# Optimization experiments

Hardware: AMD Instinct MI355X
Metric: run time of the kernel (lower is better)

## Reference

```python
import jax, jax.numpy as jnp
import numpy as np

N_GRAPHS = 2000
NODES_PER_GRAPH = 50
EDGES_PER_GRAPH = 800  # avg degree 16
N_NODES = N_GRAPHS * NODES_PER_GRAPH          # 100_000
N_EDGES = N_GRAPHS * EDGES_PER_GRAPH          # 1_600_000
F_IN, F_H, F_PRED = 64, 128, 512
N_STEPS = 3


def _glorot(key, shape):
    fan_in, fan_out = shape[0], shape[1]
    scale = jnp.sqrt(2.0 / (fan_in + fan_out)).astype(jnp.float32)
    return jax.random.normal(key, shape, dtype=jnp.float32) * scale


def setup_inputs() -> dict:
    key = jax.random.key(0)
    ks = jax.random.split(key, 12)
    node_features = jax.random.normal(ks[0], (N_NODES, F_IN), dtype=jnp.float32)
    edge_features = jax.random.normal(ks[1], (N_EDGES, 4), dtype=jnp.float32)  # unused by model
    # edges stay within their own graph: local ids in [0, NODES_PER_GRAPH) + graph offset
    offs = (jnp.arange(N_GRAPHS, dtype=jnp.int32) * NODES_PER_GRAPH)[:, None]  # [G,1]
    src = (jax.random.randint(ks[2], (N_GRAPHS, EDGES_PER_GRAPH), 0, NODES_PER_GRAPH, dtype=jnp.int32) + offs).reshape(-1)
    dst = (jax.random.randint(ks[3], (N_GRAPHS, EDGES_PER_GRAPH), 0, NODES_PER_GRAPH, dtype=jnp.int32) + offs).reshape(-1)
    pair_indices = jnp.stack([src, dst], axis=0)  # [2, E]
    num_nodes = jnp.full((N_GRAPHS,), NODES_PER_GRAPH, dtype=jnp.int32)
    num_edges = jnp.full((N_GRAPHS,), EDGES_PER_GRAPH, dtype=jnp.int32)
    # GCN weights: [F_IN->F_H, F_H->F_H, F_H->F_H]
    W0 = _glorot(ks[4], (F_IN, F_H)); b0 = jnp.zeros((F_H,), jnp.float32)
    W1 = _glorot(ks[5], (F_H, F_H)); b1 = jnp.zeros((F_H,), jnp.float32)
    W2 = _glorot(ks[6], (F_H, F_H)); b2 = jnp.zeros((F_H,), jnp.float32)
    Wp1 = _glorot(ks[7], (F_H, F_PRED)); bp1 = jnp.zeros((F_PRED,), jnp.float32)
    Wp2 = _glorot(ks[8], (F_PRED, 1)); bp2 = jnp.zeros((1,), jnp.float32)
    return dict(node_features=node_features, edge_features=edge_features,
                pair_indices=pair_indices, num_nodes=num_nodes, num_edges=num_edges,
                W0=W0, b0=b0, W1=W1, b1=b1, W2=W2, b2=b2,
                Wp1=Wp1, bp1=bp1, Wp2=Wp2, bp2=bp2)


def reference(node_features, edge_features, pair_indices, num_nodes, num_edges,
              W0, b0, W1, b1, W2, b2, Wp1, bp1, Wp2, bp2):
    N = node_features.shape[0]
    G = num_nodes.shape[0]
    src, dst = pair_indices[0], pair_indices[1]
    ones_e = jnp.ones(src.shape[0], dtype=jnp.float32)
    # DGL GraphConv norm='both': D_out^{-1/2} on source side, D_in^{-1/2} on dest side, degrees clamped >= 1
    deg_out = jax.ops.segment_sum(ones_e, src, num_segments=N)
    deg_in = jax.ops.segment_sum(ones_e, dst, num_segments=N)
    norm_out = jnp.clip(deg_out, 1.0) ** -0.5  # [N]
    norm_in = jnp.clip(deg_in, 1.0) ** -0.5    # [N]

    def gcn_conv(feat, W, b):
        h = (feat * norm_out[:, None]) @ W                       # [N, F_out] (W applied pre-aggregation)
        agg = jax.ops.segment_sum(h[src], dst, num_segments=N)   # neighbor sum
        return jax.nn.relu(agg * norm_in[:, None] + b)

    x = gcn_conv(node_features, W0, b0)
    x = gcn_conv(x, W1, b1)
    x = gcn_conv(x, W2, b2)  # [N, F_H]

    # AvgPooling: per-graph mean over nodes
    graph_ids = jnp.repeat(jnp.arange(G, dtype=jnp.int32), num_nodes, total_repeat_length=N)
    sums = jax.ops.segment_sum(x, graph_ids, num_segments=G)       # [G, F_H]
    means = sums / num_nodes.astype(x.dtype)[:, None]

    h = jax.nn.relu(means @ Wp1 + bp1)   # Dense(512, relu)
    out = h @ Wp2 + bp2                  # Dense(1, linear) -> [G, 1]
    return out
```

## Files before the change

### kernel.cpp

```cpp
#include <hip/hip_runtime.h>

#define NG   2000
#define NPG  50
#define EPG  800
#define F0   64
#define FH   128
#define FP   512

typedef __attribute__((ext_vector_type(8))) short  short8;
typedef __attribute__((ext_vector_type(8))) __bf16 bf16x8;
typedef __attribute__((ext_vector_type(4))) float  f32x4;
typedef unsigned short u16;
typedef unsigned int   u32;

__device__ inline u16 bf16_rne(float x) {
    u32 u = __builtin_bit_cast(u32, x);
    u += 0x7fffu + ((u >> 16) & 1u);
    return (u16)(u >> 16);
}
__device__ inline float bf16f(u16 h) {
    u32 u = ((u32)h) << 16;
    return __builtin_bit_cast(float, u);
}
__device__ inline u32 cvtpk2(float lo, float hi) {
    u32 r;
    asm("v_cvt_pk_bf16_f32 %0, %1, %2" : "=v"(r) : "v"(lo), "v"(hi));
    return r;
}
__device__ inline void split2(float v0, float v1, u32& hp, u32& lp) {
    hp = cvtpk2(v0, v1);
    float h0 = __builtin_bit_cast(float, hp << 16);
    float h1 = __builtin_bit_cast(float, hp & 0xffff0000u);
    lp = cvtpk2(v0 - h0, v1 - h1);
}
__device__ inline f32x4 mfma16(short8 a, short8 b, f32x4 c) {
    return __builtin_amdgcn_mfma_f32_16x16x32_bf16(
        __builtin_bit_cast(bf16x8, a), __builtin_bit_cast(bf16x8, b), c, 0, 0, 0);
}

__device__ inline int xb_idx(int row, int col) { return row * 128 + (col ^ ((row & 7) << 3)); }
__device__ inline int cn_idx(int d, int s)     { return d * 64  + (s   ^ ((d   & 7) << 3)); }

__global__ __launch_bounds__(256) void pack_w(
    const float* __restrict__ W0, const float* __restrict__ W1,
    const float* __restrict__ W2, u16* __restrict__ WpH, u16* __restrict__ WpL)
{
    int t = blockIdx.x * 256 + threadIdx.x;
    if (t >= 80 * 64) return;
    int fid = t >> 6, lane = t & 63;
    const float* W; int nsub, kstep;
    if (fid < 16)      { W = W0; int r = fid;      nsub = r >> 1; kstep = r & 1; }
    else if (fid < 48) { W = W1; int r = fid - 16; nsub = r >> 2; kstep = r & 3; }
    else               { W = W2; int r = fid - 48; nsub = r >> 2; kstep = r & 3; }
    int n  = nsub * 16 + (lane & 15);
    int kb = kstep * 32 + (lane >> 4) * 8;
    size_t off = (size_t)fid * 512 + (size_t)lane * 8;
#pragma unroll
    for (int i = 0; i < 8; ++i) {
        float v = W[(size_t)(kb + i) * FH + n];
        u16 h = bf16_rne(v);
        WpH[off + i] = h;
        WpL[off + i] = bf16_rne(v - bf16f(h));
    }
}

template<int KST, bool LAST>
__device__ void layer_fn(const u16* __restrict__ WpH, const u16* __restrict__ WpL,
                         int fid0, const float* __restrict__ bias,
                         u16* XbH, u16* XbL,
                         const short8 (&aReg)[4][2],
                         float* pool, const float* nin64, const float* nout64,
                         int lane, int nsg)
{
    const int l15 = lane & 15, lk = lane >> 4;
    const int feat = nsg * 16 + l15;
    const float bc = bias[feat];

    f32x4 acc[4];
#pragma unroll
    for (int ms = 0; ms < 4; ++ms) acc[ms] = f32x4{0.f, 0.f, 0.f, 0.f};
#pragma unroll
    for (int ks = 0; ks < KST; ++ks) {
        size_t off = (size_t)(fid0 + nsg * KST + ks) * 512 + (size_t)lane * 8;
        short8 wwh = *(const short8*)(WpH + off);
        short8 wwl = *(const short8*)(WpL + off);
        const int c0 = ks * 32 + lk * 8;
#pragma unroll
        for (int ms = 0; ms < 4; ++ms) {
            const int arow = ms * 16 + l15;
            short8 xh = *(const short8*)&XbH[xb_idx(arow, c0)];
            short8 xl = *(const short8*)&XbL[xb_idx(arow, c0)];
            acc[ms] = mfma16(xh, wwh, acc[ms]);
            acc[ms] = mfma16(xh, wwl, acc[ms]);
            acc[ms] = mfma16(xl, wwh, acc[ms]);
        }
    }
    u32 Th01[4], Th23[4], Tl01[4], Tl23[4];
#pragma unroll
    for (int ms = 0; ms < 4; ++ms) {
        const int nb = ms * 16 + lk * 4;
        float4 nq = *(const float4*)&nout64[nb];
        split2(acc[ms][0] * nq.x, acc[ms][1] * nq.y, Th01[ms], Tl01[ms]);
        split2(acc[ms][2] * nq.z, acc[ms][3] * nq.w, Th23[ms], Tl23[ms]);
    }

    const int srcA = (((lk << 1) & 3) << 4) | l15;
    const int srcB = srcA + 16;
    const bool hiMs = (lk & 2) != 0;
    short8 sbh[2], sbl[2];
#pragma unroll
    for (int ks = 0; ks < 2; ++ks) {
        u32 q0a = __shfl((int)Th01[2 * ks], srcA, 64), q0b = __shfl((int)Th01[2 * ks + 1], srcA, 64);
        u32 q1a = __shfl((int)Th23[2 * ks], srcA, 64), q1b = __shfl((int)Th23[2 * ks + 1], srcA, 64);
        u32 q2a = __shfl((int)Th01[2 * ks], srcB, 64), q2b = __shfl((int)Th01[2 * ks + 1], srcB, 64);
        u32 q3a = __shfl((int)Th23[2 * ks], srcB, 64), q3b = __shfl((int)Th23[2 * ks + 1], srcB, 64);
        uint4 qh = make_uint4(hiMs ? q0b : q0a, hiMs ? q1b : q1a,
                              hiMs ? q2b : q2a, hiMs ? q3b : q3a);
        u32 p0a = __shfl((int)Tl01[2 * ks], srcA, 64), p0b = __shfl((int)Tl01[2 * ks + 1], srcA, 64);
        u32 p1a = __shfl((int)Tl23[2 * ks], srcA, 64), p1b = __shfl((int)Tl23[2 * ks + 1], srcA, 64);
        u32 p2a = __shfl((int)Tl01[2 * ks], srcB, 64), p2b = __shfl((int)Tl01[2 * ks + 1], srcB, 64);
        u32 p3a = __shfl((int)Tl23[2 * ks], srcB, 64), p3b = __shfl((int)Tl23[2 * ks + 1], srcB, 64);
        uint4 ql = make_uint4(hiMs ? p0b : p0a, hiMs ? p1b : p1a,
                              hiMs ? p2b : p2a, hiMs ? p3b : p3a);
        sbh[ks] = __builtin_bit_cast(short8, qh);
        sbl[ks] = __builtin_bit_cast(short8, ql);
    }

    __syncthreads();

    float vs = 0.f;
#pragma unroll
    for (int ms = 0; ms < 4; ++ms) {
        f32x4 p0 = {0.f, 0.f, 0.f, 0.f}, p1 = p0;
        p0 = mfma16(aReg[ms][0], sbh[0], p0);
        p1 = mfma16(aReg[ms][1], sbh[1], p1);
        p0 = mfma16(aReg[ms][0], sbl[0], p0);
        p1 = mfma16(aReg[ms][1], sbl[1], p1);
        f32x4 a2 = p0 + p1;
        const int nb = ms * 16 + lk * 4;
        float4 ninq = *(const float4*)&nin64[nb];
        float v0 = (nb + 0 < NPG) ? fmaxf(fmaf(a2[0], ninq.x, bc), 0.f) : 0.f;
        float v1 = (nb + 1 < NPG) ? fmaxf(fmaf(a2[1], ninq.y, bc), 0.f) : 0.f;
        float v2 = (nb + 2 < NPG) ? fmaxf(fmaf(a2[2], ninq.z, bc), 0.f) : 0.f;
        float v3 = (nb + 3 < NPG) ? fmaxf(fmaf(a2[3], ninq.w, bc), 0.f) : 0.f;
        if (LAST) {
            vs += v0 + v1 + v2 + v3;
        } else {
            u32 hp01, lp01, hp23, lp23;
            split2(v0, v1, hp01, lp01);
            split2(v2, v3, hp23, lp23);
            XbH[xb_idx(nb + 0, feat)] = (u16)hp01;
            XbH[xb_idx(nb + 1, feat)] = (u16)(hp01 >> 16);
            XbH[xb_idx(nb + 2, feat)] = (u16)hp23;
            XbH[xb_idx(nb + 3, feat)] = (u16)(hp23 >> 16);
            XbL[xb_idx(nb + 0, feat)] = (u16)lp01;
            XbL[xb_idx(nb + 1, feat)] = (u16)(lp01 >> 16);
            XbL[xb_idx(nb + 2, feat)] = (u16)lp23;
            XbL[xb_idx(nb + 3, feat)] = (u16)(lp23 >> 16);
        }
    }
    if (LAST) {
        vs += __shfl_xor(vs, 16, 64);
        vs += __shfl_xor(vs, 32, 64);
        if (lane < 16) pool[feat] = vs;
    }
}

__global__ __launch_bounds__(512, 2) void gcn_fused(
    const float* __restrict__ nf, const int* __restrict__ pair,
    const float* __restrict__ b0, const float* __restrict__ b1,
    const float* __restrict__ b2,
    const u16* __restrict__ WpH, const u16* __restrict__ WpL,
    float* __restrict__ means)
{
    __shared__ u16   XbH[64 * 128], XbL[64 * 128];
    __shared__ float cnt[NPG * 64];
    __shared__ float pool[FH];
    __shared__ float nin64[64], nout64[64];

    const int tid  = threadIdx.x;
    const int g    = blockIdx.x;
    const int base = g * NPG, ebase = g * EPG;
    const int* srcp = pair;
    const int* dstp = pair + (size_t)NG * EPG;

    for (int i = tid; i < NPG * 64; i += 512) cnt[i] = 0.f;
    for (int i = 3200 + tid; i < 4096; i += 512) {
        ((u32*)XbH)[i] = 0u; ((u32*)XbL)[i] = 0u;
    }
    __syncthreads();

    for (int e = tid; e < EPG; e += 512) {
        int s = srcp[ebase + e] - base, d = dstp[ebase + e] - base;
        atomicAdd(&cnt[cn_idx(d, s)], 1.0f);
    }
    for (int i = tid; i < NPG * 16; i += 512) {
        int n = i >> 4, c4 = (i & 15) * 4;
        float4 v = *(const float4*)(nf + (size_t)(base + n) * F0 + c4);
        u32 h01, l01, h23, l23;
        split2(v.x, v.y, h01, l01);
        split2(v.z, v.w, h23, l23);
        int idx = xb_idx(n, c4);
        *(uint2*)&XbH[idx] = make_uint2(h01, h23);
        *(uint2*)&XbL[idx] = make_uint2(l01, l23);
    }
    __syncthreads();

    if (tid < 128) {
        int isOut = tid >> 6, n = tid & 63;
        if (n < NPG) {
            float s = 0.f;
            if (isOut) {
                for (int d = 0; d < NPG; ++d) s += cnt[cn_idx(d, n)];
                nout64[n] = rsqrtf(fmaxf(s, 1.f));
            } else {
                for (int c = 0; c < 64; ++c) s += cnt[n * 64 + c];
                nin64[n] = rsqrtf(fmaxf(s, 1.f));
            }
        } else {
            if (isOut) nout64[n] = 0.f; else nin64[n] = 0.f;
        }
    }
    __syncthreads();

    const int lane = tid & 63;
    const int nsg  = __builtin_amdgcn_readfirstlane(tid >> 6);
    const int l15  = lane & 15, lk = lane >> 4;

    short8 aReg[4][2];
#pragma unroll
    for (int ms = 0; ms < 4; ++ms) {
        const int d = ms * 16 + l15;
#pragma unroll
        for (int ks = 0; ks < 2; ++ks) {
            if (d < NPG) {
                int s0 = (ks * 32 + lk * 8) ^ ((d & 7) << 3);
                const float* cp = cnt + d * 64 + s0;
                float4 c0 = *(const float4*)cp;
                float4 c1 = *(const float4*)(cp + 4);
                uint4 q = make_uint4(cvtpk2(c0.x, c0.y), cvtpk2(c0.z, c0.w),
                                     cvtpk2(c1.x, c1.y), cvtpk2(c1.z, c1.w));
                aReg[ms][ks] = __builtin_bit_cast(short8, q);
            } else {
                uint4 z = make_uint4(0u, 0u, 0u, 0u);
                aReg[ms][ks] = __builtin_bit_cast(short8, z);
            }
        }
    }
    __syncthreads();

    layer_fn<2, false>(WpH, WpL, 0,  b0, XbH, XbL, aReg, pool, nin64, nout64, lane, nsg);
    __syncthreads();
    layer_fn<4, false>(WpH, WpL, 16, b1, XbH, XbL, aReg, pool, nin64, nout64, lane, nsg);
    __syncthreads();
    layer_fn<4, true >(WpH, WpL, 48, b2, XbH, XbL, aReg, pool, nin64, nout64, lane, nsg);
    __syncthreads();

    if (tid < FH) means[(size_t)g * FH + tid] = pool[tid] / (float)NPG;
}

__global__ __launch_bounds__(512) void mlp_head(
    const float* __restrict__ means, const float* __restrict__ Wp1,
    const float* __restrict__ bp1,   const float* __restrict__ Wp2,
    const float* __restrict__ bp2,   float* __restrict__ out)
{
    __shared__ float ms[8][FH];
    __shared__ float wred[8][8];
    const int tid = threadIdx.x;
    const int g0  = blockIdx.x * 8;

    for (int i = tid; i < 8 * FH; i += 512)
        ms[i >> 7][i & 127] = means[(size_t)g0 * FH + i];
    __syncthreads();

    const int f = tid;
    float acc[8];
    float bb = bp1[f];
#pragma unroll
    for (int gi = 0; gi < 8; ++gi) acc[gi] = bb;
    for (int k = 0; k < FH; ++k) {
        float w = Wp1[(size_t)k * FP + f];
#pragma unroll
        for (int gi = 0; gi < 8; ++gi) acc[gi] += ms[gi][k] * w;
    }
    float w2 = Wp2[f];
#pragma unroll
    for (int gi = 0; gi < 8; ++gi) {
        float v = fmaxf(acc[gi], 0.f) * w2;
#pragma unroll
        for (int o = 32; o > 0; o >>= 1) v += __shfl_down(v, o, 64);
        if ((tid & 63) == 0) wred[tid >> 6][gi] = v;
    }
    __syncthreads();
    if (tid < 8) {
        float s = 0.f;
#pragma unroll
        for (int w = 0; w < 8; ++w) s += wred[w][tid];
        out[g0 + tid] = s + bp2[0];
    }
}

extern "C" void kernel_launch(void* const* d_in, const int* in_sizes, int n_in,
                              void* d_out, int out_size, void* d_ws, size_t ws_size,
                              hipStream_t stream) {
    const float* nf   = (const float*)d_in[0];
    const int*   pair = (const int*)d_in[2];
    const float* W0  = (const float*)d_in[5];  const float* b0  = (const float*)d_in[6];
    const float* W1  = (const float*)d_in[7];  const float* b1  = (const float*)d_in[8];
    const float* W2  = (const float*)d_in[9];  const float* b2  = (const float*)d_in[10];
    const float* Wp1 = (const float*)d_in[11]; const float* bp1 = (const float*)d_in[12];
    const float* Wp2 = (const float*)d_in[13]; const float* bp2 = (const float*)d_in[14];

    float* means = (float*)d_ws;
    u16*   WpH   = (u16*)((char*)d_ws + (1 << 20));
    u16*   WpL   = (u16*)((char*)d_ws + (1 << 20) + 80 * 1024);
    float* out   = (float*)d_out;

    hipLaunchKernelGGL(pack_w, dim3(20), dim3(256), 0, stream, W0, W1, W2, WpH, WpL);
    hipLaunchKernelGGL(gcn_fused, dim3(NG), dim3(512), 0, stream,
                       nf, pair, b0, b1, b2, WpH, WpL, means);
    hipLaunchKernelGGL(mlp_head, dim3(NG / 8), dim3(512), 0, stream,
                       means, Wp1, bp1, Wp2, bp2, out);
}
```

Measured before the change: 92.71 us.

## Process two graphs per block and pack adjacency counts as bytes

```diff
diff --git a/kernel.cpp b/kernel.cpp
--- a/kernel.cpp
+++ b/kernel.cpp
@@ -12,6 +12,7 @@
 typedef __attribute__((ext_vector_type(4))) float  f32x4;
 typedef unsigned short u16;
 typedef unsigned int   u32;
+typedef unsigned char  u8;
 
 __device__ inline u16 bf16_rne(float x) {
     u32 u = __builtin_bit_cast(u32, x);
@@ -39,7 +40,6 @@
 }
 
 __device__ inline int xb_idx(int row, int col) { return row * 128 + (col ^ ((row & 7) << 3)); }
-__device__ inline int cn_idx(int d, int s)     { return d * 64  + (s   ^ ((d   & 7) << 3)); }
 
 __global__ __launch_bounds__(256) void pack_w(
     const float* __restrict__ W0, const float* __restrict__ W1,
@@ -67,102 +67,110 @@
 template<int KST, bool LAST>
 __device__ void layer_fn(const u16* __restrict__ WpH, const u16* __restrict__ WpL,
                          int fid0, const float* __restrict__ bias,
-                         u16* XbH, u16* XbL,
+                         u16* XbHg, u16* XbLg,
                          const short8 (&aReg)[4][2],
-                         float* pool, const float* nin64, const float* nout64,
-                         int lane, int nsg)
+                         float* poolg, const float* nin64g, const float* nout64g,
+                         int lane, int nsgPair)
 {
     const int l15 = lane & 15, lk = lane >> 4;
-    const int feat = nsg * 16 + l15;
-    const float bc = bias[feat];
-
-    f32x4 acc[4];
-#pragma unroll
-    for (int ms = 0; ms < 4; ++ms) acc[ms] = f32x4{0.f, 0.f, 0.f, 0.f};
-#pragma unroll
-    for (int ks = 0; ks < KST; ++ks) {
-        size_t off = (size_t)(fid0 + nsg * KST + ks) * 512 + (size_t)lane * 8;
-        short8 wwh = *(const short8*)(WpH + off);
-        short8 wwl = *(const short8*)(WpL + off);
-        const int c0 = ks * 32 + lk * 8;
-#pragma unroll
-        for (int ms = 0; ms < 4; ++ms) {
-            const int arow = ms * 16 + l15;
-            short8 xh = *(const short8*)&XbH[xb_idx(arow, c0)];
-            short8 xl = *(const short8*)&XbL[xb_idx(arow, c0)];
-            acc[ms] = mfma16(xh, wwh, acc[ms]);
-            acc[ms] = mfma16(xh, wwl, acc[ms]);
-            acc[ms] = mfma16(xl, wwh, acc[ms]);
-        }
-    }
-    u32 Th01[4], Th23[4], Tl01[4], Tl23[4];
-#pragma unroll
-    for (int ms = 0; ms < 4; ++ms) {
-        const int nb = ms * 16 + lk * 4;
-        float4 nq = *(const float4*)&nout64[nb];
-        split2(acc[ms][0] * nq.x, acc[ms][1] * nq.y, Th01[ms], Tl01[ms]);
-        split2(acc[ms][2] * nq.z, acc[ms][3] * nq.w, Th23[ms], Tl23[ms]);
-    }
-
     const int srcA = (((lk << 1) & 3) << 4) | l15;
     const int srcB = srcA + 16;
     const bool hiMs = (lk & 2) != 0;
-    short8 sbh[2], sbl[2];
-#pragma unroll
-    for (int ks = 0; ks < 2; ++ks) {
-        u32 q0a = __shfl((int)Th01[2 * ks], srcA, 64), q0b = __shfl((int)Th01[2 * ks + 1], srcA, 64);
-        u32 q1a = __shfl((int)Th23[2 * ks], srcA, 64), q1b = __shfl((int)Th23[2 * ks + 1], srcA, 64);
-        u32 q2a = __shfl((int)Th01[2 * ks], srcB, 64), q2b = __shfl((int)Th01[2 * ks + 1], srcB, 64);
-        u32 q3a = __shfl((int)Th23[2 * ks], srcB, 64), q3b = __shfl((int)Th23[2 * ks + 1], srcB, 64);
-        uint4 qh = make_uint4(hiMs ? q0b : q0a, hiMs ? q1b : q1a,
-                              hiMs ? q2b : q2a, hiMs ? q3b : q3a);
-        u32 p0a = __shfl((int)Tl01[2 * ks], srcA, 64), p0b = __shfl((int)Tl01[2 * ks + 1], srcA, 64);
-        u32 p1a = __shfl((int)Tl23[2 * ks], srcA, 64), p1b = __shfl((int)Tl23[2 * ks + 1], srcA, 64);
-        u32 p2a = __shfl((int)Tl01[2 * ks], srcB, 64), p2b = __shfl((int)Tl01[2 * ks + 1], srcB, 64);
-        u32 p3a = __shfl((int)Tl23[2 * ks], srcB, 64), p3b = __shfl((int)Tl23[2 * ks + 1], srcB, 64);
-        uint4 ql = make_uint4(hiMs ? p0b : p0a, hiMs ? p1b : p1a,
-                              hiMs ? p2b : p2a, hiMs ? p3b : p3a);
-        sbh[ks] = __builtin_bit_cast(short8, qh);
-        sbl[ks] = __builtin_bit_cast(short8, ql);
-    }
-
-    __syncthreads();
-
-    float vs = 0.f;
-#pragma unroll
-    for (int ms = 0; ms < 4; ++ms) {
-        f32x4 p0 = {0.f, 0.f, 0.f, 0.f}, p1 = p0;
-        p0 = mfma16(aReg[ms][0], sbh[0], p0);
-        p1 = mfma16(aReg[ms][1], sbh[1], p1);
-        p0 = mfma16(aReg[ms][0], sbl[0], p0);
-        p1 = mfma16(aReg[ms][1], sbl[1], p1);
-        f32x4 a2 = p0 + p1;
-        const int nb = ms * 16 + lk * 4;
-        float4 ninq = *(const float4*)&nin64[nb];
-        float v0 = (nb + 0 < NPG) ? fmaxf(fmaf(a2[0], ninq.x, bc), 0.f) : 0.f;
-        float v1 = (nb + 1 < NPG) ? fmaxf(fmaf(a2[1], ninq.y, bc), 0.f) : 0.f;
-        float v2 = (nb + 2 < NPG) ? fmaxf(fmaf(a2[2], ninq.z, bc), 0.f) : 0.f;
-        float v3 = (nb + 3 < NPG) ? fmaxf(fmaf(a2[3], ninq.w, bc), 0.f) : 0.f;
+
+    short8 sbh[2][2], sbl[2][2];
+
+#pragma unroll
+    for (int j = 0; j < 2; ++j) {
+        const int nsg = nsgPair * 2 + j;
+        f32x4 acc[4];
+#pragma unroll
+        for (int ms = 0; ms < 4; ++ms) acc[ms] = f32x4{0.f, 0.f, 0.f, 0.f};
+#pragma unroll
+        for (int ks = 0; ks < KST; ++ks) {
+            size_t off = (size_t)(fid0 + nsg * KST + ks) * 512 + (size_t)lane * 8;
+            short8 wwh = *(const short8*)(WpH + off);
+            short8 wwl = *(const short8*)(WpL + off);
+            const int c0 = ks * 32 + lk * 8;
+#pragma unroll
+            for (int ms = 0; ms < 4; ++ms) {
+                const int arow = ms * 16 + l15;
+                short8 xh = *(const short8*)&XbHg[xb_idx(arow, c0)];
+                short8 xl = *(const short8*)&XbLg[xb_idx(arow, c0)];
+                acc[ms] = mfma16(xh, wwh, acc[ms]);
+                acc[ms] = mfma16(xh, wwl, acc[ms]);
+                acc[ms] = mfma16(xl, wwh, acc[ms]);
+            }
+        }
+        u32 Th01[4], Th23[4], Tl01[4], Tl23[4];
+#pragma unroll
+        for (int ms = 0; ms < 4; ++ms) {
+            const int nb = ms * 16 + lk * 4;
+            float4 nq = *(const float4*)&nout64g[nb];
+            split2(acc[ms][0] * nq.x, acc[ms][1] * nq.y, Th01[ms], Tl01[ms]);
+            split2(acc[ms][2] * nq.z, acc[ms][3] * nq.w, Th23[ms], Tl23[ms]);
+        }
+#pragma unroll
+        for (int ks = 0; ks < 2; ++ks) {
+            u32 q0a = __shfl((int)Th01[2 * ks], srcA, 64), q0b = __shfl((int)Th01[2 * ks + 1], srcA, 64);
+            u32 q1a = __shfl((int)Th23[2 * ks], srcA, 64), q1b = __shfl((int)Th23[2 * ks + 1], srcA, 64);
+            u32 q2a = __shfl((int)Th01[2 * ks], srcB, 64), q2b = __shfl((int)Th01[2 * ks + 1], srcB, 64);
+            u32 q3a = __shfl((int)Th23[2 * ks], srcB, 64), q3b = __shfl((int)Th23[2 * ks + 1], srcB, 64);
+            uint4 qh = make_uint4(hiMs ? q0b : q0a, hiMs ? q1b : q1a,
+                                  hiMs ? q2b : q2a, hiMs ? q3b : q3a);
+            u32 p0a = __shfl((int)Tl01[2 * ks], srcA, 64), p0b = __shfl((int)Tl01[2 * ks + 1], srcA, 64);
+            u32 p1a = __shfl((int)Tl23[2 * ks], srcA, 64), p1b = __shfl((int)Tl23[2 * ks + 1], srcA, 64);
+            u32 p2a = __shfl((int)Tl01[2 * ks], srcB, 64), p2b = __shfl((int)Tl01[2 * ks + 1], srcB, 64);
+            u32 p3a = __shfl((int)Tl23[2 * ks], srcB, 64), p3b = __shfl((int)Tl23[2 * ks + 1], srcB, 64);
+            uint4 ql = make_uint4(hiMs ? p0b : p0a, hiMs ? p1b : p1a,
+                                  hiMs ? p2b : p2a, hiMs ? p3b : p3a);
+            sbh[j][ks] = __builtin_bit_cast(short8, qh);
+            sbl[j][ks] = __builtin_bit_cast(short8, ql);
+        }
+    }
+
+    __syncthreads();
+
+#pragma unroll
+    for (int j = 0; j < 2; ++j) {
+        const int nsg  = nsgPair * 2 + j;
+        const int feat = nsg * 16 + l15;
+        const float bc = bias[feat];
+        float vs = 0.f;
+#pragma unroll
+        for (int ms = 0; ms < 4; ++ms) {
+            f32x4 p0 = {0.f, 0.f, 0.f, 0.f}, p1 = p0;
+            p0 = mfma16(aReg[ms][0], sbh[j][0], p0);
+            p1 = mfma16(aReg[ms][1], sbh[j][1], p1);
+            p0 = mfma16(aReg[ms][0], sbl[j][0], p0);
+            p1 = mfma16(aReg[ms][1], sbl[j][1], p1);
+            f32x4 a2 = p0 + p1;
+            const int nb = ms * 16 + lk * 4;
+            float4 ninq = *(const float4*)&nin64g[nb];
+            float v0 = (nb + 0 < NPG) ? fmaxf(fmaf(a2[0], ninq.x, bc), 0.f) : 0.f;
+            float v1 = (nb + 1 < NPG) ? fmaxf(fmaf(a2[1], ninq.y, bc), 0.f) : 0.f;
+            float v2 = (nb + 2 < NPG) ? fmaxf(fmaf(a2[2], ninq.z, bc), 0.f) : 0.f;
+            float v3 = (nb + 3 < NPG) ? fmaxf(fmaf(a2[3], ninq.w, bc), 0.f) : 0.f;
+            if (LAST) {
+                vs += v0 + v1 + v2 + v3;
+            } else {
+                u32 hp01, lp01, hp23, lp23;
+                split2(v0, v1, hp01, lp01);
+                split2(v2, v3, hp23, lp23);
+                XbHg[xb_idx(nb + 0, feat)] = (u16)hp01;
+                XbHg[xb_idx(nb + 1, feat)] = (u16)(hp01 >> 16);
+                XbHg[xb_idx(nb + 2, feat)] = (u16)hp23;
+                XbHg[xb_idx(nb + 3, feat)] = (u16)(hp23 >> 16);
+                XbLg[xb_idx(nb + 0, feat)] = (u16)lp01;
+                XbLg[xb_idx(nb + 1, feat)] = (u16)(lp01 >> 16);
+                XbLg[xb_idx(nb + 2, feat)] = (u16)lp23;
+                XbLg[xb_idx(nb + 3, feat)] = (u16)(lp23 >> 16);
+            }
+        }
         if (LAST) {
-            vs += v0 + v1 + v2 + v3;
-        } else {
-            u32 hp01, lp01, hp23, lp23;
-            split2(v0, v1, hp01, lp01);
-            split2(v2, v3, hp23, lp23);
-            XbH[xb_idx(nb + 0, feat)] = (u16)hp01;
-            XbH[xb_idx(nb + 1, feat)] = (u16)(hp01 >> 16);
-            XbH[xb_idx(nb + 2, feat)] = (u16)hp23;
-            XbH[xb_idx(nb + 3, feat)] = (u16)(hp23 >> 16);
-            XbL[xb_idx(nb + 0, feat)] = (u16)lp01;
-            XbL[xb_idx(nb + 1, feat)] = (u16)(lp01 >> 16);
-            XbL[xb_idx(nb + 2, feat)] = (u16)lp23;
-            XbL[xb_idx(nb + 3, feat)] = (u16)(lp23 >> 16);
-        }
-    }
-    if (LAST) {
-        vs += __shfl_xor(vs, 16, 64);
-        vs += __shfl_xor(vs, 32, 64);
-        if (lane < 16) pool[feat] = vs;
+            vs += __shfl_xor(vs, 16, 64);
+            vs += __shfl_xor(vs, 32, 64);
+            if (lane < 16) poolg[feat] = vs;
+        }
     }
 }
 
@@ -173,59 +181,83 @@
     const u16* __restrict__ WpH, const u16* __restrict__ WpL,
     float* __restrict__ means)
 {
-    __shared__ u16   XbH[64 * 128], XbL[64 * 128];
-    __shared__ float cnt[NPG * 64];
-    __shared__ float pool[FH];
-    __shared__ float nin64[64], nout64[64];
-
-    const int tid  = threadIdx.x;
-    const int g    = blockIdx.x;
-    const int base = g * NPG, ebase = g * EPG;
+    __shared__ u16 XbH[2 * 64 * 128], XbL[2 * 64 * 128];
+    __shared__ u8  cnt8[2 * NPG * 64];
+    __shared__ float pool[2 * FH];
+    __shared__ float nin64[2 * 64], nout64[2 * 64];
+
+    const int tid   = threadIdx.x;
+    const int g     = blockIdx.x;
+    const int base  = g * 2 * NPG;
+    const int ebase = g * 2 * EPG;
     const int* srcp = pair;
     const int* dstp = pair + (size_t)NG * EPG;
-
-    for (int i = tid; i < NPG * 64; i += 512) cnt[i] = 0.f;
-    for (int i = 3200 + tid; i < 4096; i += 512) {
-        ((u32*)XbH)[i] = 0u; ((u32*)XbL)[i] = 0u;
-    }
-    __syncthreads();
-
-    for (int e = tid; e < EPG; e += 512) {
-        int s = srcp[ebase + e] - base, d = dstp[ebase + e] - base;
-        atomicAdd(&cnt[cn_idx(d, s)], 1.0f);
-    }
-    for (int i = tid; i < NPG * 16; i += 512) {
-        int n = i >> 4, c4 = (i & 15) * 4;
-        float4 v = *(const float4*)(nf + (size_t)(base + n) * F0 + c4);
+    u32* cw = (u32*)cnt8;
+
+    for (int i = tid; i < 1600; i += 512) cw[i] = 0u;
+    for (int i = tid; i < 1792; i += 512) {
+        int gi = i / 896, k = 3200 + (i - gi * 896);
+        ((u32*)XbH)[gi * 4096 + k] = 0u;
+        ((u32*)XbL)[gi * 4096 + k] = 0u;
+    }
+    __syncthreads();
+
+    for (int e = tid; e < 2 * EPG; e += 512) {
+        int gi = (e >= EPG);
+        int gb = base + gi * NPG;
+        int s = srcp[ebase + e] - gb;
+        int d = dstp[ebase + e] - gb;
+        atomicAdd(&cw[gi * 800 + d * 16 + (s >> 2)], 1u << (8 * (s & 3)));
+    }
+    for (int i = tid; i < 2 * NPG * 16; i += 512) {
+        int gi = (i >= NPG * 16);
+        int r  = i - gi * NPG * 16;
+        int n = r >> 4, c4 = (r & 15) * 4;
+        float4 v = *(const float4*)(nf + (size_t)(base + gi * NPG + n) * F0 + c4);
         u32 h01, l01, h23, l23;
         split2(v.x, v.y, h01, l01);
         split2(v.z, v.w, h23, l23);
-        int idx = xb_idx(n, c4);
+        int idx = gi * 8192 + xb_idx(n, c4);
         *(uint2*)&XbH[idx] = make_uint2(h01, h23);
         *(uint2*)&XbL[idx] = make_uint2(l01, l23);
     }
     __syncthreads();
 
-    if (tid < 128) {
-        int isOut = tid >> 6, n = tid & 63;
+    if (tid < 256) {
+        int gi = tid >> 7, isOut = (tid >> 6) & 1, n = tid & 63;
+        const u8* c8 = cnt8 + gi * 3200;
         if (n < NPG) {
-            float s = 0.f;
             if (isOut) {
-                for (int d = 0; d < NPG; ++d) s += cnt[cn_idx(d, n)];
-                nout64[n] = rsqrtf(fmaxf(s, 1.f));
+                float s = 0.f;
+                for (int d = 0; d < NPG; ++d) s += (float)c8[d * 64 + n];
+                nout64[gi * 64 + n] = rsqrtf(fmaxf(s, 1.f));
             } else {
-                for (int c = 0; c < 64; ++c) s += cnt[n * 64 + c];
-                nin64[n] = rsqrtf(fmaxf(s, 1.f));
+                u32 a = 0;
+                const u32* w = (const u32*)(c8 + n * 64);
+                for (int k = 0; k < 16; ++k) {
+                    u32 x = w[k];
+                    a += (x & 255) + ((x >> 8) & 255) + ((x >> 16) & 255) + (x >> 24);
+                }
+                nin64[gi * 64 + n] = rsqrtf(fmaxf((float)a, 1.f));
             }
         } else {
-            if (isOut) nout64[n] = 0.f; else nin64[n] = 0.f;
-        }
-    }
-    __syncthreads();
-
-    const int lane = tid & 63;
-    const int nsg  = __builtin_amdgcn_readfirstlane(tid >> 6);
-    const int l15  = lane & 15, lk = lane >> 4;
+            if (isOut) nout64[gi * 64 + n] = 0.f; else nin64[gi * 64 + n] = 0.f;
+        }
+    }
+    __syncthreads();
+
+    const int lane    = tid & 63;
+    const int wv      = __builtin_amdgcn_readfirstlane(tid >> 6);
+    const int gid     = wv >> 2;
+    const int nsgPair = wv & 3;
+    const int l15 = lane & 15, lk = lane >> 4;
+
+    u16* XbHg = XbH + gid * 8192;
+    u16* XbLg = XbL + gid * 8192;
+    const float* nin64g  = nin64  + gid * 64;
+    const float* nout64g = nout64 + gid * 64;
+    float* poolg = pool + gid * FH;
+    const u8* c8 = cnt8 + gid * 3200;
 
     short8 aReg[4][2];
 #pragma unroll
@@ -234,12 +266,13 @@
 #pragma unroll
         for (int ks = 0; ks < 2; ++ks) {
             if (d < NPG) {
-                int s0 = (ks * 32 + lk * 8) ^ ((d & 7) << 3);
-                const float* cp = cnt + d * 64 + s0;
-                float4 c0 = *(const float4*)cp;
-                float4 c1 = *(const float4*)(cp + 4);
-                uint4 q = make_uint4(cvtpk2(c0.x, c0.y), cvtpk2(c0.z, c0.w),
-                                     cvtpk2(c1.x, c1.y), cvtpk2(c1.z, c1.w));
+                const u32* wp = (const u32*)(c8 + d * 64 + ks * 32 + lk * 8);
+                u32 w0 = wp[0], w1 = wp[1];
+                uint4 q = make_uint4(
+                    cvtpk2((float)(w0 & 255), (float)((w0 >> 8) & 255)),
+                    cvtpk2((float)((w0 >> 16) & 255), (float)(w0 >> 24)),
+                    cvtpk2((float)(w1 & 255), (float)((w1 >> 8) & 255)),
+                    cvtpk2((float)((w1 >> 16) & 255), (float)(w1 >> 24)));
                 aReg[ms][ks] = __builtin_bit_cast(short8, q);
             } else {
                 uint4 z = make_uint4(0u, 0u, 0u, 0u);
@@ -247,16 +280,16 @@
             }
         }
     }
-    __syncthreads();
-
-    layer_fn<2, false>(WpH, WpL, 0,  b0, XbH, XbL, aReg, pool, nin64, nout64, lane, nsg);
-    __syncthreads();
-    layer_fn<4, false>(WpH, WpL, 16, b1, XbH, XbL, aReg, pool, nin64, nout64, lane, nsg);
-    __syncthreads();
-    layer_fn<4, true >(WpH, WpL, 48, b2, XbH, XbL, aReg, pool, nin64, nout64, lane, nsg);
-    __syncthreads();
-
-    if (tid < FH) means[(size_t)g * FH + tid] = pool[tid] / (float)NPG;
+
+    layer_fn<2, false>(WpH, WpL, 0,  b0, XbHg, XbLg, aReg, poolg, nin64g, nout64g, lane, nsgPair);
+    __syncthreads();
+    layer_fn<4, false>(WpH, WpL, 16, b1, XbHg, XbLg, aReg, poolg, nin64g, nout64g, lane, nsgPair);
+    __syncthreads();
+    layer_fn<4, true >(WpH, WpL, 48, b2, XbHg, XbLg, aReg, poolg, nin64g, nout64g, lane, nsgPair);
+    __syncthreads();
+
+    if (tid < 2 * FH)
+        means[(size_t)(2 * g + (tid >> 7)) * FH + (tid & 127)] = pool[tid] / (float)NPG;
 }
 
 __global__ __launch_bounds__(512) void mlp_head(
@@ -317,7 +350,7 @@
     float* out   = (float*)d_out;
 
     hipLaunchKernelGGL(pack_w, dim3(20), dim3(256), 0, stream, W0, W1, W2, WpH, WpL);
-    hipLaunchKernelGGL(gcn_fused, dim3(NG), dim3(512), 0, stream,
+    hipLaunchKernelGGL(gcn_fused, dim3(NG / 2), dim3(512), 0, stream,
                        nf, pair, b0, b1, b2, WpH, WpL, means);
     hipLaunchKernelGGL(mlp_head, dim3(NG / 8), dim3(512), 0, stream,
                        means, Wp1, bp1, Wp2, bp2, out);
```

Measured after the change: 91.61 us. Within noise of the previous version (-1.2%).
